# Optimization experiments

Measured on AMD Instinct MI355X. Metric: run time of the kernel, lower is better.

Reference implementation:

```python
import jax, jax.numpy as jnp
import numpy as np

NHEADS = 16
KVHEADS = 4
HEAD_DIM = 128  # emb_kq_per_head == emb_v_per_head
ROPE_THETA = 10000.0


def _rotary(x, cos, sin):
    # x: [B, S, H, D]; half-split rotation
    x1, x2 = jnp.split(x, 2, axis=-1)
    rot = jnp.concatenate([-x2, x1], axis=-1)
    return x * cos + rot * sin


def setup_inputs() -> dict:
    key = jax.random.key(0)
    k1, k2, k3 = jax.random.split(key, 3)
    B, S, E = 2, 2048, 2048
    qkv_out = NHEADS * HEAD_DIM + 2 * KVHEADS * HEAD_DIM  # 3072
    return {
        "x": jax.random.normal(k1, (B, S, E), dtype=jnp.float32),
        "w_qkv": jax.random.normal(k2, (E, qkv_out), dtype=jnp.float32) * 0.02,
        "w_dense": jax.random.normal(k3, (NHEADS * HEAD_DIM, E), dtype=jnp.float32) * 0.02,
    }


def reference(x, w_qkv, w_dense):
    B, S, E = x.shape
    D = HEAD_DIM
    # fused QKV projection (use_bias=False), then split per FusedQKV.splits
    qkv = x @ w_qkv  # [B, S, 3072]
    q, k, v = jnp.split(qkv, [NHEADS * D, NHEADS * D + KVHEADS * D], axis=-1)
    q = q.reshape(B, S, NHEADS, D)
    k = k.reshape(B, S, KVHEADS, D)
    v = v.reshape(B, S, KVHEADS, D)

    # rotary position encoding, positions = arange(S)
    pos = jnp.arange(S, dtype=jnp.float32)
    inv_freq = 1.0 / (ROPE_THETA ** (jnp.arange(0, D, 2, dtype=jnp.float32) / D))
    ang = pos[:, None] * inv_freq[None, :]                 # [S, D/2]
    ang = jnp.concatenate([ang, ang], axis=-1)             # [S, D]
    cos = jnp.cos(ang)[None, :, None, :]                   # [1, S, 1, D]
    sin = jnp.sin(ang)[None, :, None, :]
    q = _rotary(q, cos, sin)
    k = _rotary(k, cos, sin)

    # GQA: expand kv heads to query heads
    rep = NHEADS // KVHEADS
    k = jnp.repeat(k, rep, axis=2)  # [B, S, NHEADS, D]
    v = jnp.repeat(v, rep, axis=2)

    scale = 1.0 / jnp.sqrt(jnp.asarray(D, dtype=x.dtype))
    scores = jnp.einsum("bqhd,bkhd->bhqk", q, k) * scale   # [B, H, S, S]
    causal = jnp.tril(jnp.ones((S, S), dtype=bool))
    scores = jnp.where(causal[None, None], scores, jnp.finfo(scores.dtype).min)
    probs = jax.nn.softmax(scores, axis=-1)
    attn = jnp.einsum("bhqk,bkhd->bqhd", probs, v)         # [B, S, H, D]
    attn = attn.reshape(B, S, NHEADS * D)
    return attn @ w_dense                                  # [B, S, E]
```

## Files before the change

kernel.cpp:

```cpp
#include <hip/hip_runtime.h>
#include <type_traits>


typedef __attribute__((ext_vector_type(8))) short short8;
typedef __attribute__((ext_vector_type(4))) float floatx4;
typedef __attribute__((ext_vector_type(4))) unsigned short ushort4v;

constexpr int NH    = 16;
constexpr int NKV   = 4;
constexpr int HD    = 128;
constexpr int SEQ   = 2048;
constexpr int EMB   = 2048;
constexpr int NBATCH = 2;
constexpr int MROWS = NBATCH * SEQ;
constexpr int NQKV  = (NH + 2 * NKV) * HD;

__device__ __forceinline__ unsigned short f2b(float f) {
  union { float f; unsigned u; } v; v.f = f;
  unsigned u = v.u + 0x7FFFu + ((v.u >> 16) & 1u);
  return (unsigned short)(u >> 16);
}
__device__ __forceinline__ float b2f(unsigned short h) {
  union { unsigned u; float f; } v; v.u = (unsigned)h << 16;
  return v.f;
}

__device__ __forceinline__ void gload_lds16(const unsigned short* g,
                                            unsigned short* lds) {
  __builtin_amdgcn_global_load_lds(
      (const __attribute__((address_space(1))) unsigned int*)g,
      (__attribute__((address_space(3))) unsigned int*)lds, 16, 0, 0);
}

__global__ void cvt_f32_bf16(const float* __restrict__ in,
                             unsigned short* __restrict__ out, int n) {
  int i = (blockIdx.x * 256 + threadIdx.x) * 4;
  if (i + 3 < n) {
    floatx4 v = *(const floatx4*)(in + i);
    ushort4v o = { f2b(v[0]), f2b(v[1]), f2b(v[2]), f2b(v[3]) };
    *(ushort4v*)(out + i) = o;
  }
}

__global__ void transpose_cvt_dual(const float* __restrict__ wqkv,
                                   unsigned short* __restrict__ oqkv,
                                   const float* __restrict__ wd,
                                   unsigned short* __restrict__ od) {
  const int z = blockIdx.z;
  const float* in = z ? wd : wqkv;
  unsigned short* out = z ? od : oqkv;
  const int R = EMB;
  const int C = z ? EMB : NQKV;
  int c0 = blockIdx.x * 32, r0 = blockIdx.y * 32;
  if (c0 >= C) return;
  __shared__ float t[32][33];
  int tx = threadIdx.x & 31, ty = threadIdx.x >> 5;
#pragma unroll
  for (int i = 0; i < 32; i += 8)
    t[ty + i][tx] = in[(long)(r0 + ty + i) * C + (c0 + tx)];
  __syncthreads();
#pragma unroll
  for (int i = 0; i < 32; i += 8)
    out[(long)(c0 + ty + i) * R + (r0 + tx)] = f2b(t[tx][ty + i]);
}

__global__ void rope_kernel(unsigned short* __restrict__ Qb,
                            unsigned short* __restrict__ Kb, float qscale) {
  int idx = blockIdx.x * 256 + threadIdx.x;
  int i = idx & 63;
  int s = (idx >> 6) & (SEQ - 1);
  int bh = idx >> 17;
  unsigned short* p;
  float scale;
  if (bh < NBATCH * NH) { p = Qb + ((long)bh * SEQ + s) * HD; scale = qscale; }
  else { p = Kb + ((long)(bh - NBATCH * NH) * SEQ + s) * HD; scale = 1.0f; }
  float e = -(float)i * (2.0f * 13.287712379549449f / 128.0f);
  float ang = (float)s * exp2f(e);
  float sn, c;
  sincosf(ang, &sn, &c);
  float x1 = b2f(p[i]), x2 = b2f(p[i + 64]);
  p[i]      = f2b((x1 * c - x2 * sn) * scale);
  p[i + 64] = f2b((x2 * c + x1 * sn) * scale);
}

constexpr int BM = 128, BN = 128, BK = 64;

template <int MODE>
__global__ __launch_bounds__(256, 3) void gemm_bt(
    const unsigned short* __restrict__ A,
    const unsigned short* __restrict__ BT,
    int Mdim, int Ndim, int Kdim,
    float* __restrict__ outF,
    unsigned short* __restrict__ Qb,
    unsigned short* __restrict__ Kb,
    unsigned short* __restrict__ Vt) {
  __shared__ __align__(16) unsigned short smem[BM * BK + BN * BK];
  unsigned short (*As)[BK] = (unsigned short (*)[BK])smem;
  unsigned short (*Bs)[BK] = (unsigned short (*)[BK])(smem + BM * BK);
  const int tid = threadIdx.x;
  const int bm = blockIdx.y * BM;
  const int bn = blockIdx.x * BN;
  const int wave = tid >> 6, lane = tid & 63;
  const int l = lane & 15, q = lane >> 4;
  const int l7 = l & 7;
  const int wm = (wave >> 1) * 64, wn = (wave & 1) * 64;

  floatx4 acc[4][4] = {};

  const int srow = lane >> 3;
  const int scol = ((lane & 7) ^ srow) * 8;
  const unsigned short* Arow = A + (long)bm * Kdim;
  const unsigned short* Brow = BT + (long)bn * Kdim;

  for (int k0 = 0; k0 < Kdim; k0 += BK) {
#pragma unroll
    for (int i = 0; i < 4; ++i) {
      const int r0 = wave * 32 + i * 8;
      gload_lds16(Arow + (long)(r0 + srow) * Kdim + k0 + scol, &As[r0][0]);
      gload_lds16(Brow + (long)(r0 + srow) * Kdim + k0 + scol, &Bs[r0][0]);
    }
    __syncthreads();
#pragma unroll
    for (int kk = 0; kk < 2; ++kk) {
      short8 af[4], bfr[4];
#pragma unroll
      for (int mi = 0; mi < 4; ++mi)
        af[mi] = *(const short8*)&As[wm + mi * 16 + l][((kk * 4 + q) ^ l7) * 8];
#pragma unroll
      for (int ni = 0; ni < 4; ++ni)
        bfr[ni] = *(const short8*)&Bs[wn + ni * 16 + l][((kk * 4 + q) ^ l7) * 8];
#pragma unroll
      for (int mi = 0; mi < 4; ++mi)
#pragma unroll
        for (int ni = 0; ni < 4; ++ni)
          acc[mi][ni] = __builtin_amdgcn_mfma_f32_16x16x32_bf16(
              af[mi], bfr[ni], acc[mi][ni], 0, 0, 0);
    }
    __syncthreads();
  }

  if constexpr (MODE == 1) {
#pragma unroll
    for (int mi = 0; mi < 4; ++mi) {
      const int rowbase = bm + wm + mi * 16 + q * 4;
#pragma unroll
      for (int ni = 0; ni < 4; ++ni) {
        const int col = bn + wn + ni * 16 + l;
#pragma unroll
        for (int r = 0; r < 4; ++r)
          outF[(long)(rowbase + r) * Ndim + col] = acc[mi][ni][r];
      }
    }
  } else if (bn >= (NH + NKV) * HD) {
    const int hh = (bn - (NH + NKV) * HD) >> 7;
#pragma unroll
    for (int mi = 0; mi < 4; ++mi) {
      const int m0 = bm + wm + mi * 16 + q * 4;
      const int bb = m0 >> 11, s = m0 & (SEQ - 1);
      unsigned short* vtb = Vt + ((long)(bb * NKV + hh)) * HD * SEQ;
#pragma unroll
      for (int ni = 0; ni < 4; ++ni) {
        const int d = wn + ni * 16 + l;
        ushort4v pv = { f2b(acc[mi][ni][0]), f2b(acc[mi][ni][1]),
                        f2b(acc[mi][ni][2]), f2b(acc[mi][ni][3]) };
        *(ushort4v*)(vtb + (long)d * SEQ + s) = pv;
      }
    }
  } else {
    unsigned short (*Ct)[128] = (unsigned short (*)[128])smem;
#pragma unroll
    for (int mi = 0; mi < 4; ++mi)
#pragma unroll
      for (int ni = 0; ni < 4; ++ni)
#pragma unroll
        for (int r = 0; r < 4; ++r) {
          const int row = wm + mi * 16 + q * 4 + r;
          const int col = wn + ni * 16 + l;
          const int cs = ((((col >> 3) ^ row) & 7) | (col & 64 ? 8 : 0)) * 8 + (col & 7);
          Ct[row][cs] = f2b(acc[mi][ni][r]);
        }
    __syncthreads();
    const int row = tid >> 1, g = tid & 1;
    const int m = bm + row, bb = m >> 11, s = m & (SEQ - 1);
    unsigned short* dst;
    if (bn < NH * HD)
      dst = Qb + (((long)(bb * NH + (bn >> 7))) * SEQ + s) * HD;
    else
      dst = Kb + (((long)(bb * NKV + ((bn - NH * HD) >> 7))) * SEQ + s) * HD;
#pragma unroll
    for (int i = 0; i < 8; ++i) {
      const int blk = (g * 8) + (i ^ (row & 7));
      *(short8*)(dst + g * 64 + i * 8) = *(const short8*)&Ct[row][blk * 8];
    }
  }
}

__global__ __launch_bounds__(256, 2) void attn_kernel(
    const unsigned short* __restrict__ Q,
    const unsigned short* __restrict__ K,
    const unsigned short* __restrict__ VT,
    unsigned short* __restrict__ attn) {
  const int h = blockIdx.y, b = blockIdx.z;
  const int t = b ? (15 - (int)blockIdx.x) : (int)blockIdx.x;
  const int kvh = h >> 2;
  const int tid = threadIdx.x;
  const int wave = tid >> 6, lane = tid & 63;
  const int l = lane & 15, q = lane >> 4;
  const int l7 = l & 7;
  const int wq = wave * 32;

  const unsigned short* Kh  = K  + ((long)(b * NKV + kvh)) * SEQ * HD;
  const unsigned short* VTh = VT + ((long)(b * NKV + kvh)) * HD * SEQ;

  __shared__ __align__(16) unsigned short Ks[2][64 * 128];
  __shared__ __align__(16) unsigned short VTs[2][128 * 64];
  __shared__ __align__(16) unsigned short Ps[128 * 64];

  int koff[4], voff[4];
  {
    const int k_rl = lane >> 4, k_bp = lane & 15;
    const int v_rl = lane >> 3, v_bp = lane & 7;
#pragma unroll
    for (int j = 0; j < 4; ++j) {
      const int rk = (wave * 4 + j) * 4 + k_rl;
      koff[j] = rk * HD + (k_bp ^ (rk & 15)) * 8;
      const int rv = (wave * 4 + j) * 8 + v_rl;
      voff[j] = rv * SEQ + (v_bp ^ (rv & 7)) * 8;
    }
  }

  short8 onesf;
#pragma unroll
  for (int i = 0; i < 8; ++i) onesf[i] = (short)0x3F80;

  auto stage = [&](int c, int buf) {
    const unsigned short* kc = Kh + c * (64 * HD);
    const unsigned short* vc = VTh + c * 64;
#pragma unroll
    for (int j = 0; j < 4; ++j)
      gload_lds16(kc + koff[j], &Ks[buf][(wave * 4 + j) * 4 * 128]);
#pragma unroll
    for (int j = 0; j < 4; ++j)
      gload_lds16(vc + voff[j], &VTs[buf][(wave * 4 + j) * 8 * 64]);
  };

  const unsigned short* Qh = Q + (((long)(b * NH + h)) * SEQ + t * 128) * HD;
  short8 qf[2][4];
#pragma unroll
  for (int mh = 0; mh < 2; ++mh)
#pragma unroll
    for (int kk = 0; kk < 4; ++kk)
      qf[mh][kk] = *(const short8*)(Qh + (long)(wq + mh * 16 + l) * HD + kk * 32 + q * 8);

  floatx4 o[2][9] = {};

  auto chunk_body = [&](auto masked, int cur, int kv0) {
    constexpr bool MASKED = decltype(masked)::value;
    floatx4 sf[2][4] = {};
#pragma unroll
    for (int kk = 0; kk < 4; ++kk) {
      short8 kf[4];
#pragma unroll
      for (int ni = 0; ni < 4; ++ni)
        kf[ni] = *(const short8*)&Ks[cur][(ni * 16 + l) * 128 + (((kk * 4 + q) ^ l) * 8)];
#pragma unroll
      for (int mh = 0; mh < 2; ++mh)
#pragma unroll
        for (int ni = 0; ni < 4; ++ni)
          sf[mh][ni] = __builtin_amdgcn_mfma_f32_16x16x32_bf16(
              kf[ni], qf[mh][kk], sf[mh][ni], 0, 0, 0);
    }
#pragma unroll
    for (int mh = 0; mh < 2; ++mh) {
      const int prow = wq + mh * 16 + l;
      const int qrow = t * 128 + prow;
#pragma unroll
      for (int ni = 0; ni < 4; ++ni) {
        if constexpr (MASKED) {
#pragma unroll
          for (int r = 0; r < 4; ++r)
            if (kv0 + ni * 16 + q * 4 + r > qrow) sf[mh][ni][r] = -3e38f;
        }
        float e0 = exp2f(sf[mh][ni][0]);
        float e1 = exp2f(sf[mh][ni][1]);
        float e2 = exp2f(sf[mh][ni][2]);
        float e3 = exp2f(sf[mh][ni][3]);
        unsigned u0, u1;
        asm("v_cvt_pk_bf16_f32 %0, %1, %2" : "=v"(u0) : "v"(e0), "v"(e1));
        asm("v_cvt_pk_bf16_f32 %0, %1, %2" : "=v"(u1) : "v"(e2), "v"(e3));
        const int base = prow * 64 + (((ni * 2 + (q >> 1)) ^ l7) * 8) + (q & 1) * 4;
        *(unsigned*)&Ps[base] = u0;
        *(unsigned*)&Ps[base + 2] = u1;
      }
    }
#pragma unroll
    for (int kvk = 0; kvk < 2; ++kvk) {
      const int pb = ((kvk * 4 + q) ^ l7) * 8;
      short8 pf0 = *(const short8*)&Ps[(wq + l) * 64 + pb];
      short8 pf1 = *(const short8*)&Ps[(wq + 16 + l) * 64 + pb];
#pragma unroll
      for (int di = 0; di < 8; ++di) {
        short8 vf = *(const short8*)&VTs[cur][(di * 16 + l) * 64 + pb];
        o[0][di] = __builtin_amdgcn_mfma_f32_16x16x32_bf16(pf0, vf, o[0][di], 0, 0, 0);
        o[1][di] = __builtin_amdgcn_mfma_f32_16x16x32_bf16(pf1, vf, o[1][di], 0, 0, 0);
      }
      o[0][8] = __builtin_amdgcn_mfma_f32_16x16x32_bf16(pf0, onesf, o[0][8], 0, 0, 0);
      o[1][8] = __builtin_amdgcn_mfma_f32_16x16x32_bf16(pf1, onesf, o[1][8], 0, 0, 0);
    }
  };

  const int nc = 2 * t + 2;
  stage(0, 0);
  __syncthreads();

  int c = 0;
#pragma unroll 1
  for (; c < nc - 2; ++c) {
    stage(c + 1, (c & 1) ^ 1);
    chunk_body(std::false_type{}, c & 1, c * 64);
    __syncthreads();
  }
  stage(c + 1, (c & 1) ^ 1);
  chunk_body(std::true_type{}, c & 1, c * 64);
  __syncthreads();
  ++c;
  chunk_body(std::true_type{}, c & 1, c * 64);
  __syncthreads();

  unsigned short (*Ob)[136] = (unsigned short (*)[136])&Ks[0][0];
#pragma unroll
  for (int mh = 0; mh < 2; ++mh)
#pragma unroll
    for (int r = 0; r < 4; ++r) {
      const float inv = 1.0f / o[mh][8][r];
#pragma unroll
      for (int di = 0; di < 8; ++di)
        Ob[wq + mh * 16 + q * 4 + r][di * 16 + l] = f2b(o[mh][di][r] * inv);
    }
  __syncthreads();
  {
    const int row = tid >> 1, g = (tid & 1) * 64;
    const int s = t * 128 + row;
    unsigned short* dst = attn + ((long)(b * SEQ + s)) * (NH * HD) + h * HD + g;
#pragma unroll
    for (int j = 0; j < 8; ++j)
      *(short8*)(dst + j * 8) = *(const short8*)&Ob[row][g + j * 8];
  }
}

extern "C" void kernel_launch(void* const* d_in, const int* in_sizes, int n_in,
                              void* d_out, int out_size, void* d_ws, size_t ws_size,
                              hipStream_t stream) {
  const float* x       = (const float*)d_in[0];
  const float* w_qkv   = (const float*)d_in[1];
  const float* w_dense = (const float*)d_in[2];
  float* out = (float*)d_out;

  char* ws = (char*)d_ws;
  const size_t MB = 1024 * 1024;
  unsigned short* xb    = (unsigned short*)(ws);
  unsigned short* wqkvT = (unsigned short*)(ws + 16 * MB);
  unsigned short* wdT   = (unsigned short*)(ws + 28 * MB);
  unsigned short* Qb    = (unsigned short*)(ws + 36 * MB);
  unsigned short* Kb    = (unsigned short*)(ws + 52 * MB);
  unsigned short* VTb   = (unsigned short*)(ws + 56 * MB);
  unsigned short* attn  = xb;

  const float qscale = 0.08838834764831845f * 1.4426950408889634f;

  cvt_f32_bf16<<<(MROWS * EMB) / (256 * 4), 256, 0, stream>>>(x, xb, MROWS * EMB);
  transpose_cvt_dual<<<dim3(NQKV / 32, EMB / 32, 2), 256, 0, stream>>>(
      w_qkv, wqkvT, w_dense, wdT);

  gemm_bt<0><<<dim3(NQKV / BN, MROWS / BM), 256, 0, stream>>>(
      xb, wqkvT, MROWS, NQKV, EMB, nullptr, Qb, Kb, VTb);

  rope_kernel<<<(NBATCH * (NH + NKV) * SEQ * 64) / 256, 256, 0, stream>>>(Qb, Kb, qscale);

  attn_kernel<<<dim3(16, NH, NBATCH), 256, 0, stream>>>(Qb, Kb, VTb, attn);

  gemm_bt<1><<<dim3(EMB / BN, MROWS / BM), 256, 0, stream>>>(
      attn, wdT, MROWS, EMB, NH * HD, out, nullptr, nullptr, nullptr);
}
```

Before: 301.8 us.

## Keep softmax probabilities in registers by permuting V sequence layout to match MFMA

The QKV GEMM epilogue now writes V^T with the sequence index permuted inside each 64-wide block, so the score MFMA output layout already matches the A-operand layout of the PV MFMA. The attention kernel packs the bf16 probabilities straight into register fragments instead of writing them to LDS and reading them back, and drops the Ps shared buffer. This removes LDS traffic and shrinks shared memory per block. It relies on the V producer and consumer agreeing on the permutation.

```diff
diff --git a/kernel.cpp b/kernel.cpp
--- a/kernel.cpp
+++ b/kernel.cpp
@@ -5,6 +5,7 @@
 typedef __attribute__((ext_vector_type(8))) short short8;
 typedef __attribute__((ext_vector_type(4))) float floatx4;
 typedef __attribute__((ext_vector_type(4))) unsigned short ushort4v;
+typedef __attribute__((ext_vector_type(4))) unsigned int uint4v;
 
 constexpr int NH    = 16;
 constexpr int NKV   = 4;
@@ -157,13 +158,16 @@
     for (int mi = 0; mi < 4; ++mi) {
       const int m0 = bm + wm + mi * 16 + q * 4;
       const int bb = m0 >> 11, s = m0 & (SEQ - 1);
+      const int s6 = s & 63;
+      const int p6 = (s6 & 32) | ((s6 & 12) << 1) | ((s6 & 16) >> 2);
+      const int sp = (s & ~63) | p6;
       unsigned short* vtb = Vt + ((long)(bb * NKV + hh)) * HD * SEQ;
 #pragma unroll
       for (int ni = 0; ni < 4; ++ni) {
         const int d = wn + ni * 16 + l;
         ushort4v pv = { f2b(acc[mi][ni][0]), f2b(acc[mi][ni][1]),
                         f2b(acc[mi][ni][2]), f2b(acc[mi][ni][3]) };
-        *(ushort4v*)(vtb + (long)d * SEQ + s) = pv;
+        *(ushort4v*)(vtb + (long)d * SEQ + sp) = pv;
       }
     }
   } else {
@@ -212,9 +216,9 @@
   const unsigned short* Kh  = K  + ((long)(b * NKV + kvh)) * SEQ * HD;
   const unsigned short* VTh = VT + ((long)(b * NKV + kvh)) * HD * SEQ;
 
-  __shared__ __align__(16) unsigned short Ks[2][64 * 128];
-  __shared__ __align__(16) unsigned short VTs[2][128 * 64];
-  __shared__ __align__(16) unsigned short Ps[128 * 64];
+  __shared__ __align__(16) unsigned short smem[2 * 64 * 128 + 2 * 128 * 64];
+  unsigned short (*Ks)[64 * 128]  = (unsigned short (*)[64 * 128])smem;
+  unsigned short (*VTs)[128 * 64] = (unsigned short (*)[128 * 64])(smem + 2 * 64 * 128);
 
   int koff[4], voff[4];
   {
@@ -270,10 +274,11 @@
           sf[mh][ni] = __builtin_amdgcn_mfma_f32_16x16x32_bf16(
               kf[ni], qf[mh][kk], sf[mh][ni], 0, 0, 0);
     }
+    short8 pf[2][2];
 #pragma unroll
     for (int mh = 0; mh < 2; ++mh) {
-      const int prow = wq + mh * 16 + l;
-      const int qrow = t * 128 + prow;
+      const int qrow = t * 128 + wq + mh * 16 + l;
+      unsigned u[8];
 #pragma unroll
       for (int ni = 0; ni < 4; ++ni) {
         if constexpr (MASKED) {
@@ -285,27 +290,26 @@
         float e1 = exp2f(sf[mh][ni][1]);
         float e2 = exp2f(sf[mh][ni][2]);
         float e3 = exp2f(sf[mh][ni][3]);
-        unsigned u0, u1;
-        asm("v_cvt_pk_bf16_f32 %0, %1, %2" : "=v"(u0) : "v"(e0), "v"(e1));
-        asm("v_cvt_pk_bf16_f32 %0, %1, %2" : "=v"(u1) : "v"(e2), "v"(e3));
-        const int base = prow * 64 + (((ni * 2 + (q >> 1)) ^ l7) * 8) + (q & 1) * 4;
-        *(unsigned*)&Ps[base] = u0;
-        *(unsigned*)&Ps[base + 2] = u1;
+        asm("v_cvt_pk_bf16_f32 %0, %1, %2" : "=v"(u[ni * 2]) : "v"(e0), "v"(e1));
+        asm("v_cvt_pk_bf16_f32 %0, %1, %2" : "=v"(u[ni * 2 + 1]) : "v"(e2), "v"(e3));
       }
-    }
-#pragma unroll
-    for (int kvk = 0; kvk < 2; ++kvk) {
-      const int pb = ((kvk * 4 + q) ^ l7) * 8;
-      short8 pf0 = *(const short8*)&Ps[(wq + l) * 64 + pb];
-      short8 pf1 = *(const short8*)&Ps[(wq + 16 + l) * 64 + pb];
+      union { uint4v v; short8 s; } a0, a1;
+      a0.v = (uint4v){u[0], u[1], u[2], u[3]};
+      a1.v = (uint4v){u[4], u[5], u[6], u[7]};
+      pf[mh][0] = a0.s;
+      pf[mh][1] = a1.s;
+    }
+#pragma unroll
+    for (int c2 = 0; c2 < 2; ++c2) {
+      const int pb = ((c2 * 4 + q) ^ l7) * 8;
 #pragma unroll
       for (int di = 0; di < 8; ++di) {
         short8 vf = *(const short8*)&VTs[cur][(di * 16 + l) * 64 + pb];
-        o[0][di] = __builtin_amdgcn_mfma_f32_16x16x32_bf16(pf0, vf, o[0][di], 0, 0, 0);
-        o[1][di] = __builtin_amdgcn_mfma_f32_16x16x32_bf16(pf1, vf, o[1][di], 0, 0, 0);
+        o[0][di] = __builtin_amdgcn_mfma_f32_16x16x32_bf16(pf[0][c2], vf, o[0][di], 0, 0, 0);
+        o[1][di] = __builtin_amdgcn_mfma_f32_16x16x32_bf16(pf[1][c2], vf, o[1][di], 0, 0, 0);
       }
-      o[0][8] = __builtin_amdgcn_mfma_f32_16x16x32_bf16(pf0, onesf, o[0][8], 0, 0, 0);
-      o[1][8] = __builtin_amdgcn_mfma_f32_16x16x32_bf16(pf1, onesf, o[1][8], 0, 0, 0);
+      o[0][8] = __builtin_amdgcn_mfma_f32_16x16x32_bf16(pf[0][c2], onesf, o[0][8], 0, 0, 0);
+      o[1][8] = __builtin_amdgcn_mfma_f32_16x16x32_bf16(pf[1][c2], onesf, o[1][8], 0, 0, 0);
     }
   };
 
@@ -327,7 +331,7 @@
   chunk_body(std::true_type{}, c & 1, c * 64);
   __syncthreads();
 
-  unsigned short (*Ob)[136] = (unsigned short (*)[136])&Ks[0][0];
+  unsigned short (*Ob)[136] = (unsigned short (*)[136])smem;
 #pragma unroll
   for (int mh = 0; mh < 2; ++mh)
 #pragma unroll
```

Result: faster. 283.0 us (-6.2%).
